# Kernel optimization log

Hardware: AMD Instinct MI355X
Metric: run time of the kernel (lower is better)

The kernel has to match this reference:

```python
import jax, jax.numpy as jnp
import numpy as np

N_NODES = 100000
N_EDGES = 800000
NUM_FEATURES = 64
HIDDEN = 16
N_GRAPHS = 64


def setup_inputs() -> dict:
    key = jax.random.key(0)
    ks = jax.random.split(key, 12)
    x = jax.random.normal(ks[0], (N_NODES, NUM_FEATURES), dtype=jnp.float32)
    edge_index = jax.random.randint(ks[1], (2, N_EDGES), 0, N_NODES, dtype=jnp.int64)
    batch = jnp.sort(jax.random.randint(ks[2], (N_NODES,), 0, N_GRAPHS, dtype=jnp.int64))
    def glorot(k, shape):
        fan_in, fan_out = shape
        s = jnp.sqrt(2.0 / (fan_in + fan_out))
        return jax.random.normal(k, shape, dtype=jnp.float32) * s
    return {
        "x": x,
        "edge_index": edge_index,
        "batch": batch,
        "W1_rel": glorot(ks[3], (NUM_FEATURES, HIDDEN)),
        "W1_root": glorot(ks[4], (NUM_FEATURES, HIDDEN)),
        "b1": jnp.zeros((HIDDEN,), dtype=jnp.float32),
        "W2_rel": glorot(ks[5], (HIDDEN, HIDDEN)),
        "W2_root": glorot(ks[6], (HIDDEN, HIDDEN)),
        "b2": jnp.zeros((HIDDEN,), dtype=jnp.float32),
        "Wlin": glorot(ks[7], (HIDDEN, 1)),
        "blin": jnp.zeros((1,), dtype=jnp.float32),
    }


def _graph_conv(h, src, dst, W_rel, W_root, b):
    # PyG GraphConv: out_i = W_rel @ sum_{j->i} h_j + b + W_root @ h_i
    agg = jax.ops.segment_sum(h[src], dst, num_segments=h.shape[0])
    return agg @ W_rel + b + h @ W_root


def reference(x, edge_index, batch, W1_rel, W1_root, b1, W2_rel, W2_root, b2, Wlin, blin):
    src, dst = edge_index[0], edge_index[1]
    h = jax.nn.relu(_graph_conv(x, src, dst, W1_rel, W1_root, b1))
    # F.dropout(training=False) is identity at inference
    h = _graph_conv(h, src, dst, W2_rel, W2_root, b2)
    # global mean pool over graphs
    sums = jax.ops.segment_sum(h, batch, num_segments=N_GRAPHS)  # [G, H]
    counts = jax.ops.segment_sum(jnp.ones((h.shape[0],), dtype=h.dtype), batch, num_segments=N_GRAPHS)
    pooled = sums / jnp.maximum(counts, 1.0)[:, None]
    out = pooled @ Wlin + blin  # [G, 1]
    return out.squeeze(1)
```

## Files before the change

kernel.cpp:

```cpp
#include <hip/hip_runtime.h>

#define BUCKET_BITS 7
#define BUCKET_N    128
#define SEG_CAP     1280
#define EPB         4096
#define EPT         16
#define OVF_CAP     16384
#define MAXBUCK     1024

__global__ void k_init(int* __restrict__ cursor, int* __restrict__ ovf_n,
                       float* __restrict__ T1, float* __restrict__ T2,
                       float* __restrict__ cntg, int nbuck, int n_graphs)
{
    const int t = threadIdx.x;
    for (int i = t; i < nbuck; i += 1024) cursor[i * 16] = i * SEG_CAP;
    if (t < n_graphs) { T1[t] = 0.f; T2[t] = 0.f; cntg[t] = 0.f; }
    if (t == 0) *ovf_n = 0;
}

__global__ __launch_bounds__(256) void k_scatter_bin(
    const int* __restrict__ src, const int* __restrict__ dst,
    int* __restrict__ cursor, int2* __restrict__ seg,
    int* __restrict__ ovf_n, int2* __restrict__ ovf,
    int n_edges, int nbuck)
{
    __shared__ int hist[MAXBUCK];
    __shared__ int base[MAXBUCK];
    const int t = threadIdx.x;
    for (int i = t; i < nbuck; i += 256) hist[i] = 0;
    __syncthreads();

    const int e0 = blockIdx.x * EPB;
    int es[EPT], ed[EPT], ep[EPT];
#pragma unroll
    for (int k = 0; k < EPT; ++k) {
        const int e = e0 + k * 256 + t;
        if (e < n_edges) {
            ed[k] = dst[e];
            es[k] = src[e];
            ep[k] = atomicAdd(&hist[ed[k] >> BUCKET_BITS], 1);
        } else ed[k] = -1;
    }
    __syncthreads();
    for (int b = t; b < nbuck; b += 256) {
        const int h = hist[b];
        base[b] = h ? atomicAdd(&cursor[b * 16], h) : 0;
    }
    __syncthreads();
#pragma unroll
    for (int k = 0; k < EPT; ++k) {
        if (ed[k] >= 0) {
            const int b = ed[k] >> BUCKET_BITS;
            const int addr = base[b] + ep[k];
            if (addr < (b + 1) * SEG_CAP) {
                seg[addr] = make_int2(es[k], ed[k]);
            } else {
                const int op = atomicAdd(ovf_n, 1);
                if (op < OVF_CAP) ovf[op] = make_int2(es[k], ed[k]);
            }
        }
    }
}

__global__ __launch_bounds__(256) void k_transform1(
    const float* __restrict__ x, const float* __restrict__ Wrel,
    const float* __restrict__ Wroot, const float* __restrict__ bias,
    float* __restrict__ p1, float* __restrict__ r1, int n_nodes)
{
    __shared__ float s_x[64 * 68];
    __shared__ float s_wrT[16 * 68];
    __shared__ float s_woT[16 * 68];
    __shared__ float s_b[16];

    const int t = threadIdx.x;
    for (int i = t; i < 1024; i += 256) {
        const int k = i >> 4, o = i & 15;
        s_wrT[o * 68 + k] = Wrel[i];
        s_woT[o * 68 + k] = Wroot[i];
    }
    if (t < 16) s_b[t] = bias[t];

    const int node0 = blockIdx.x * 64;
    for (int i = t; i < 1024; i += 256) {
        const int r = i >> 4, c = i & 15;
        const int node = node0 + r;
        if (node < n_nodes)
            *(float4*)&s_x[r * 68 + c * 4] =
                *(const float4*)(x + (size_t)node * 64 + c * 4);
    }
    __syncthreads();

    const int o = t & 15, ng = t >> 4;
    float accr[4] = {0.f, 0.f, 0.f, 0.f};
    float acco[4] = {0.f, 0.f, 0.f, 0.f};
#pragma unroll
    for (int k4 = 0; k4 < 16; ++k4) {
        const float4 wr = *(const float4*)&s_wrT[o * 68 + k4 * 4];
        const float4 wo = *(const float4*)&s_woT[o * 68 + k4 * 4];
#pragma unroll
        for (int j = 0; j < 4; ++j) {
            const float4 xv = *(const float4*)&s_x[(ng * 4 + j) * 68 + k4 * 4];
            accr[j] = fmaf(xv.x, wr.x, fmaf(xv.y, wr.y, fmaf(xv.z, wr.z, fmaf(xv.w, wr.w, accr[j]))));
            acco[j] = fmaf(xv.x, wo.x, fmaf(xv.y, wo.y, fmaf(xv.z, wo.z, fmaf(xv.w, wo.w, acco[j]))));
        }
    }
#pragma unroll
    for (int j = 0; j < 4; ++j) {
        const int node = node0 + ng * 4 + j;
        if (node < n_nodes) {
            p1[(size_t)node * 16 + o] = accr[j];
            r1[(size_t)node * 16 + o] = acco[j] + s_b[o];
        }
    }
}

__global__ __launch_bounds__(256) void k_aggregate(
    const float* __restrict__ p1, const float* __restrict__ r1,
    const int2* __restrict__ seg, const int* __restrict__ cursor,
    const int* __restrict__ ovf_n, const int2* __restrict__ ovf,
    const int* __restrict__ batch,
    const float* __restrict__ W2rel, const float* __restrict__ W2root,
    const float* __restrict__ Wlin,
    float* __restrict__ s_out, float* __restrict__ T2, float* __restrict__ cntg,
    int* __restrict__ g_sorted, int* __restrict__ g_beg, int* __restrict__ g_cnt,
    int n_nodes)
{
    __shared__ int s_src[SEG_CAP];
    __shared__ int hist[BUCKET_N];
    __shared__ int iscan[BUCKET_N];
    __shared__ int cur[BUCKET_N];
    __shared__ float s_w2r[16], s_w2o[16];
    __shared__ float sT2[64], scnt[64];
    __shared__ int s_no;

    const int t = threadIdx.x, b = blockIdx.x;
    if (t < BUCKET_N) hist[t] = 0;
    if (t < 16) {
        float ar = 0.f, ao = 0.f;
#pragma unroll
        for (int o = 0; o < 16; ++o) {
            const float wl = Wlin[o];
            ar = fmaf(W2rel[t * 16 + o], wl, ar);
            ao = fmaf(W2root[t * 16 + o], wl, ao);
        }
        s_w2r[t] = ar; s_w2o[t] = ao;
    }
    if (t < 64) { sT2[t] = 0.f; scnt[t] = 0.f; }
    if (t == 0) s_no = min(*ovf_n, OVF_CAP);
    __syncthreads();

    const int bstart = b * SEG_CAP;
    const int count = min(cursor[b * 16] - bstart, SEG_CAP);

    for (int i = t; i < count; i += 256)
        atomicAdd(&hist[seg[bstart + i].y & (BUCKET_N - 1)], 1);
    __syncthreads();
    if (t < BUCKET_N) iscan[t] = hist[t];
    __syncthreads();
    for (int off = 1; off < BUCKET_N; off <<= 1) {
        int x = 0;
        if (t < BUCKET_N) { x = iscan[t]; if (t >= off) x += iscan[t - off]; }
        __syncthreads();
        if (t < BUCKET_N) iscan[t] = x;
        __syncthreads();
    }
    if (t < BUCKET_N) cur[t] = iscan[t] - hist[t];
    __syncthreads();
    for (int i = t; i < count; i += 256) {
        const int2 e = seg[bstart + i];
        const int l = e.y & (BUCKET_N - 1);
        s_src[atomicAdd(&cur[l], 1)] = e.x;
    }
    __syncthreads();

    for (int i = t; i < count; i += 256) g_sorted[bstart + i] = s_src[i];
    if (t < BUCKET_N) {
        const int nodew = b * BUCKET_N + t;
        if (nodew < n_nodes) {
            g_beg[nodew] = bstart + iscan[t] - hist[t];
            g_cnt[nodew] = hist[t];
        }
    }

    const int nl = t >> 1, half = t & 1;
    const int node = b * BUCKET_N + nl;
    if (node < n_nodes) {
        const int end = iscan[nl];
        const int beg = end - hist[nl];
        float4 acc0 = make_float4(0.f, 0.f, 0.f, 0.f);
        float4 acc1 = make_float4(0.f, 0.f, 0.f, 0.f);
        int j = beg;
        for (; j + 2 <= end; j += 2) {
            const int s0 = s_src[j], s1 = s_src[j + 1];
            const float4* q0 = (const float4*)(p1 + (size_t)s0 * 16 + half * 8);
            const float4* q1 = (const float4*)(p1 + (size_t)s1 * 16 + half * 8);
            const float4 a0 = q0[0], a1 = q0[1], b0 = q1[0], b1 = q1[1];
            acc0.x += a0.x + b0.x; acc0.y += a0.y + b0.y;
            acc0.z += a0.z + b0.z; acc0.w += a0.w + b0.w;
            acc1.x += a1.x + b1.x; acc1.y += a1.y + b1.y;
            acc1.z += a1.z + b1.z; acc1.w += a1.w + b1.w;
        }
        if (j < end) {
            const int s0 = s_src[j];
            const float4* q0 = (const float4*)(p1 + (size_t)s0 * 16 + half * 8);
            const float4 a0 = q0[0], a1 = q0[1];
            acc0.x += a0.x; acc0.y += a0.y; acc0.z += a0.z; acc0.w += a0.w;
            acc1.x += a1.x; acc1.y += a1.y; acc1.z += a1.z; acc1.w += a1.w;
        }
        for (int ov = 0; ov < s_no; ++ov) {
            const int2 e = ovf[ov];
            if (e.y == node) {
                const float4* q0 = (const float4*)(p1 + (size_t)e.x * 16 + half * 8);
                const float4 a0 = q0[0], a1 = q0[1];
                acc0.x += a0.x; acc0.y += a0.y; acc0.z += a0.z; acc0.w += a0.w;
                acc1.x += a1.x; acc1.y += a1.y; acc1.z += a1.z; acc1.w += a1.w;
            }
        }
        const float4 rA = *(const float4*)(r1 + (size_t)node * 16 + half * 8);
        const float4 rB = *(const float4*)(r1 + (size_t)node * 16 + half * 8 + 4);
        float4 h0, h1;
        h0.x = fmaxf(acc0.x + rA.x, 0.f); h0.y = fmaxf(acc0.y + rA.y, 0.f);
        h0.z = fmaxf(acc0.z + rA.z, 0.f); h0.w = fmaxf(acc0.w + rA.w, 0.f);
        h1.x = fmaxf(acc1.x + rB.x, 0.f); h1.y = fmaxf(acc1.y + rB.y, 0.f);
        h1.z = fmaxf(acc1.z + rB.z, 0.f); h1.w = fmaxf(acc1.w + rB.w, 0.f);
        const float4 w0r = *(const float4*)&s_w2r[half * 8];
        const float4 w1r = *(const float4*)&s_w2r[half * 8 + 4];
        const float4 w0o = *(const float4*)&s_w2o[half * 8];
        const float4 w1o = *(const float4*)&s_w2o[half * 8 + 4];
        float ps = h0.x * w0r.x + h0.y * w0r.y + h0.z * w0r.z + h0.w * w0r.w
                 + h1.x * w1r.x + h1.y * w1r.y + h1.z * w1r.z + h1.w * w1r.w;
        float pu = h0.x * w0o.x + h0.y * w0o.y + h0.z * w0o.z + h0.w * w0o.w
                 + h1.x * w1o.x + h1.y * w1o.y + h1.z * w1o.z + h1.w * w1o.w;
        ps += __shfl_xor(ps, 1);
        pu += __shfl_xor(pu, 1);
        if (half == 0) {
            s_out[node] = ps;
            const int g = batch[node];
            atomicAdd(&sT2[g], pu);
            atomicAdd(&scnt[g], 1.f);
        }
    }
    __syncthreads();
    if (t < 64) {
        if (sT2[t] != 0.f) unsafeAtomicAdd(&T2[t], sT2[t]);
        if (scnt[t] != 0.f) unsafeAtomicAdd(&cntg[t], scnt[t]);
    }
}

__global__ __launch_bounds__(256) void k_T1(
    const float* __restrict__ s_in, const int* __restrict__ g_sorted,
    const int* __restrict__ g_beg, const int* __restrict__ g_cnt,
    const int* __restrict__ batch,
    const int* __restrict__ ovf_n, const int2* __restrict__ ovf,
    float* __restrict__ T1, int n_nodes)
{
    __shared__ float bins[64];
    const int t = threadIdx.x;
    if (t < 64) bins[t] = 0.f;
    __syncthreads();

    const int node = blockIdx.x * 256 + t;
    if (node < n_nodes) {
        const int beg = g_beg[node], c = g_cnt[node];
        float acc = 0.f;
        int j = 0;
        for (; j + 4 <= c; j += 4) {
            const int a = g_sorted[beg + j],     b2 = g_sorted[beg + j + 1];
            const int cc = g_sorted[beg + j + 2], d = g_sorted[beg + j + 3];
            acc += s_in[a] + s_in[b2] + s_in[cc] + s_in[d];
        }
        for (; j < c; ++j) acc += s_in[g_sorted[beg + j]];
        if (acc != 0.f) atomicAdd(&bins[batch[node]], acc);
    }
    __syncthreads();
    if (t < 64 && bins[t] != 0.f) unsafeAtomicAdd(&T1[t], bins[t]);

    if (blockIdx.x == 0) {
        const int n = min(*ovf_n, OVF_CAP);
        for (int i = t; i < n; i += 256)
            unsafeAtomicAdd(&T1[batch[ovf[i].y]], s_in[ovf[i].x]);
    }
}

__global__ void k_finalize(
    const float* __restrict__ T1, const float* __restrict__ T2,
    const float* __restrict__ cntg, const float* __restrict__ b2,
    const float* __restrict__ Wlin, const float* __restrict__ blin,
    float* __restrict__ out, int n_graphs)
{
    const int g = threadIdx.x;
    if (g >= n_graphs) return;
    float cb = 0.f;
#pragma unroll
    for (int o = 0; o < 16; ++o) cb = fmaf(b2[o], Wlin[o], cb);
    const float c = fmaxf(cntg[g], 1.f);
    out[g] = (T1[g] + T2[g]) / c + cb + blin[0];
}

extern "C" void kernel_launch(void* const* d_in, const int* in_sizes, int n_in,
                              void* d_out, int out_size, void* d_ws, size_t ws_size,
                              hipStream_t stream) {
    const float* x       = (const float*)d_in[0];
    const int*   ei      = (const int*)d_in[1];
    const int*   batch   = (const int*)d_in[2];
    const float* W1_rel  = (const float*)d_in[3];
    const float* W1_root = (const float*)d_in[4];
    const float* b1      = (const float*)d_in[5];
    const float* W2_rel  = (const float*)d_in[6];
    const float* W2_root = (const float*)d_in[7];
    const float* b2      = (const float*)d_in[8];
    const float* Wlin    = (const float*)d_in[9];
    const float* blin    = (const float*)d_in[10];
    float* out = (float*)d_out;

    const int N = in_sizes[0] / 64;
    const int E = in_sizes[1] / 2;
    const int G = out_size;
    const int nbuck = (N + BUCKET_N - 1) >> BUCKET_BITS;

    const int* src = ei;
    const int* dst = ei + E;

    auto rnd4 = [](size_t v) { return (v + 3) & ~(size_t)3; };
    float* ws = (float*)d_ws;
    size_t off = 0;
    float* p1       = ws + off; off += rnd4((size_t)N * 16);
    float* r1       = ws + off; off += rnd4((size_t)N * 16);
    float* s_buf    = ws + off; off += rnd4((size_t)N);
    int*   cursor   = (int*)(ws + off); off += rnd4((size_t)nbuck * 16);
    int2*  seg      = (int2*)(ws + off); off += rnd4((size_t)nbuck * SEG_CAP * 2);
    int*   g_sorted = (int*)(ws + off); off += rnd4((size_t)nbuck * SEG_CAP);
    int*   g_beg    = (int*)(ws + off); off += rnd4((size_t)N);
    int*   g_cnt    = (int*)(ws + off); off += rnd4((size_t)N);
    int2*  ovf      = (int2*)(ws + off); off += rnd4((size_t)OVF_CAP * 2);
    int*   ovf_n    = (int*)(ws + off); off += 4;
    float* T1       = ws + off; off += rnd4((size_t)G);
    float* T2       = ws + off; off += rnd4((size_t)G);
    float* cntg     = ws + off; off += rnd4((size_t)G);

    const int sb = (E + EPB - 1) / EPB;
    const int tb = (N + 63) / 64;
    const int ab = (N + 255) / 256;

    k_init       <<<1, 1024, 0, stream>>>(cursor, ovf_n, T1, T2, cntg, nbuck, G);
    k_scatter_bin<<<sb, 256, 0, stream>>>(src, dst, cursor, seg, ovf_n, ovf, E, nbuck);
    k_transform1 <<<tb, 256, 0, stream>>>(x, W1_rel, W1_root, b1, p1, r1, N);
    k_aggregate  <<<nbuck, 256, 0, stream>>>(p1, r1, seg, cursor, ovf_n, ovf, batch,
                                             W2_rel, W2_root, Wlin, s_buf, T2, cntg,
                                             g_sorted, g_beg, g_cnt, N);
    k_T1         <<<ab, 256, 0, stream>>>(s_buf, g_sorted, g_beg, g_cnt, batch,
                                          ovf_n, ovf, T1, N);
    k_finalize   <<<1, 64, 0, stream>>>(T1, T2, cntg, b2, Wlin, blin, out, G);
}
```

Measured before the change: 169.3 us.

## Store projected features in fp16, cache edges in registers, use wave-shuffle scan

The projected layer-1 features p1 are now stored as half precision, which halves the bytes of the random gather in the aggregation kernel, and are widened to fp32 for accumulation. The aggregation kernel also keeps its edges in registers between the histogram and placement passes, avoiding a second read of the segment. It replaces the shared-memory Hillis-Steele scan with a wavefront shuffle scan. The init kernel is split across 8 blocks. fp16 rounding of p1 adds numerical error to the result.

```diff
diff --git a/kernel.cpp b/kernel.cpp
--- a/kernel.cpp
+++ b/kernel.cpp
@@ -1,4 +1,5 @@
 #include <hip/hip_runtime.h>
+#include <hip/hip_fp16.h>
 
 #define BUCKET_BITS 7
 #define BUCKET_N    128
@@ -8,14 +9,18 @@
 #define OVF_CAP     16384
 #define MAXBUCK     1024
 
-__global__ void k_init(int* __restrict__ cursor, int* __restrict__ ovf_n,
-                       float* __restrict__ T1, float* __restrict__ T2,
-                       float* __restrict__ cntg, int nbuck, int n_graphs)
-{
-    const int t = threadIdx.x;
-    for (int i = t; i < nbuck; i += 1024) cursor[i * 16] = i * SEG_CAP;
-    if (t < n_graphs) { T1[t] = 0.f; T2[t] = 0.f; cntg[t] = 0.f; }
-    if (t == 0) *ovf_n = 0;
+__global__ __launch_bounds__(256) void k_init(
+    int* __restrict__ cursor, int* __restrict__ ovf_n,
+    float* __restrict__ T1, float* __restrict__ T2,
+    float* __restrict__ cntg, int nbuck, int n_graphs)
+{
+    const int i0 = blockIdx.x * 256 + threadIdx.x;
+    for (int i = i0; i < nbuck; i += gridDim.x * 256) cursor[i * 16] = i * SEG_CAP;
+    if (blockIdx.x == 0) {
+        const int t = threadIdx.x;
+        if (t < n_graphs) { T1[t] = 0.f; T2[t] = 0.f; cntg[t] = 0.f; }
+        if (t == 0) *ovf_n = 0;
+    }
 }
 
 __global__ __launch_bounds__(256) void k_scatter_bin(
@@ -65,7 +70,7 @@
 __global__ __launch_bounds__(256) void k_transform1(
     const float* __restrict__ x, const float* __restrict__ Wrel,
     const float* __restrict__ Wroot, const float* __restrict__ bias,
-    float* __restrict__ p1, float* __restrict__ r1, int n_nodes)
+    __half* __restrict__ p1, float* __restrict__ r1, int n_nodes)
 {
     __shared__ float s_x[64 * 68];
     __shared__ float s_wrT[16 * 68];
@@ -108,14 +113,24 @@
     for (int j = 0; j < 4; ++j) {
         const int node = node0 + ng * 4 + j;
         if (node < n_nodes) {
-            p1[(size_t)node * 16 + o] = accr[j];
+            p1[(size_t)node * 16 + o] = __float2half(accr[j]);
             r1[(size_t)node * 16 + o] = acco[j] + s_b[o];
         }
     }
 }
 
+__device__ inline void acc_half8(float* acc, uint4 raw) {
+    const __half2* h2 = (const __half2*)&raw;
+#pragma unroll
+    for (int k = 0; k < 4; ++k) {
+        const float2 f = __half22float2(h2[k]);
+        acc[2 * k]     += f.x;
+        acc[2 * k + 1] += f.y;
+    }
+}
+
 __global__ __launch_bounds__(256) void k_aggregate(
-    const float* __restrict__ p1, const float* __restrict__ r1,
+    const __half* __restrict__ p1, const float* __restrict__ r1,
     const int2* __restrict__ seg, const int* __restrict__ cursor,
     const int* __restrict__ ovf_n, const int2* __restrict__ ovf,
     const int* __restrict__ batch,
@@ -131,7 +146,7 @@
     __shared__ int cur[BUCKET_N];
     __shared__ float s_w2r[16], s_w2o[16];
     __shared__ float sT2[64], scnt[64];
-    __shared__ int s_no;
+    __shared__ int s_no, s_w0;
 
     const int t = threadIdx.x, b = blockIdx.x;
     if (t < BUCKET_N) hist[t] = 0;
@@ -152,25 +167,33 @@
     const int bstart = b * SEG_CAP;
     const int count = min(cursor[b * 16] - bstart, SEG_CAP);
 
-    for (int i = t; i < count; i += 256)
-        atomicAdd(&hist[seg[bstart + i].y & (BUCKET_N - 1)], 1);
-    __syncthreads();
-    if (t < BUCKET_N) iscan[t] = hist[t];
-    __syncthreads();
-    for (int off = 1; off < BUCKET_N; off <<= 1) {
-        int x = 0;
-        if (t < BUCKET_N) { x = iscan[t]; if (t >= off) x += iscan[t - off]; }
-        __syncthreads();
-        if (t < BUCKET_N) iscan[t] = x;
-        __syncthreads();
-    }
-    if (t < BUCKET_N) cur[t] = iscan[t] - hist[t];
-    __syncthreads();
+    int2 er[5];
+    int ne = 0;
     for (int i = t; i < count; i += 256) {
-        const int2 e = seg[bstart + i];
-        const int l = e.y & (BUCKET_N - 1);
-        s_src[atomicAdd(&cur[l], 1)] = e.x;
-    }
+        er[ne] = seg[bstart + i];
+        atomicAdd(&hist[er[ne].y & (BUCKET_N - 1)], 1);
+        ++ne;
+    }
+    __syncthreads();
+    int v = 0;
+    if (t < BUCKET_N) {
+        v = hist[t];
+#pragma unroll
+        for (int off = 1; off < 64; off <<= 1) {
+            const int u = __shfl_up(v, off);
+            if ((t & 63) >= off) v += u;
+        }
+        if (t == 63) s_w0 = v;
+    }
+    __syncthreads();
+    if (t < BUCKET_N) {
+        if (t >= 64) v += s_w0;
+        iscan[t] = v;
+        cur[t] = v - hist[t];
+    }
+    __syncthreads();
+    for (int k = 0; k < ne; ++k)
+        s_src[atomicAdd(&cur[er[k].y & (BUCKET_N - 1)], 1)] = er[k].x;
     __syncthreads();
 
     for (int i = t; i < count; i += 256) g_sorted[bstart + i] = s_src[i];
@@ -187,50 +210,39 @@
     if (node < n_nodes) {
         const int end = iscan[nl];
         const int beg = end - hist[nl];
-        float4 acc0 = make_float4(0.f, 0.f, 0.f, 0.f);
-        float4 acc1 = make_float4(0.f, 0.f, 0.f, 0.f);
+        float acc[8] = {0.f, 0.f, 0.f, 0.f, 0.f, 0.f, 0.f, 0.f};
         int j = beg;
         for (; j + 2 <= end; j += 2) {
             const int s0 = s_src[j], s1 = s_src[j + 1];
-            const float4* q0 = (const float4*)(p1 + (size_t)s0 * 16 + half * 8);
-            const float4* q1 = (const float4*)(p1 + (size_t)s1 * 16 + half * 8);
-            const float4 a0 = q0[0], a1 = q0[1], b0 = q1[0], b1 = q1[1];
-            acc0.x += a0.x + b0.x; acc0.y += a0.y + b0.y;
-            acc0.z += a0.z + b0.z; acc0.w += a0.w + b0.w;
-            acc1.x += a1.x + b1.x; acc1.y += a1.y + b1.y;
-            acc1.z += a1.z + b1.z; acc1.w += a1.w + b1.w;
+            const uint4 a = *(const uint4*)(p1 + (size_t)s0 * 16 + half * 8);
+            const uint4 c = *(const uint4*)(p1 + (size_t)s1 * 16 + half * 8);
+            acc_half8(acc, a);
+            acc_half8(acc, c);
         }
         if (j < end) {
-            const int s0 = s_src[j];
-            const float4* q0 = (const float4*)(p1 + (size_t)s0 * 16 + half * 8);
-            const float4 a0 = q0[0], a1 = q0[1];
-            acc0.x += a0.x; acc0.y += a0.y; acc0.z += a0.z; acc0.w += a0.w;
-            acc1.x += a1.x; acc1.y += a1.y; acc1.z += a1.z; acc1.w += a1.w;
+            const uint4 a = *(const uint4*)(p1 + (size_t)s_src[j] * 16 + half * 8);
+            acc_half8(acc, a);
         }
         for (int ov = 0; ov < s_no; ++ov) {
             const int2 e = ovf[ov];
             if (e.y == node) {
-                const float4* q0 = (const float4*)(p1 + (size_t)e.x * 16 + half * 8);
-                const float4 a0 = q0[0], a1 = q0[1];
-                acc0.x += a0.x; acc0.y += a0.y; acc0.z += a0.z; acc0.w += a0.w;
-                acc1.x += a1.x; acc1.y += a1.y; acc1.z += a1.z; acc1.w += a1.w;
+                const uint4 a = *(const uint4*)(p1 + (size_t)e.x * 16 + half * 8);
+                acc_half8(acc, a);
             }
         }
         const float4 rA = *(const float4*)(r1 + (size_t)node * 16 + half * 8);
         const float4 rB = *(const float4*)(r1 + (size_t)node * 16 + half * 8 + 4);
-        float4 h0, h1;
-        h0.x = fmaxf(acc0.x + rA.x, 0.f); h0.y = fmaxf(acc0.y + rA.y, 0.f);
-        h0.z = fmaxf(acc0.z + rA.z, 0.f); h0.w = fmaxf(acc0.w + rA.w, 0.f);
-        h1.x = fmaxf(acc1.x + rB.x, 0.f); h1.y = fmaxf(acc1.y + rB.y, 0.f);
-        h1.z = fmaxf(acc1.z + rB.z, 0.f); h1.w = fmaxf(acc1.w + rB.w, 0.f);
-        const float4 w0r = *(const float4*)&s_w2r[half * 8];
-        const float4 w1r = *(const float4*)&s_w2r[half * 8 + 4];
-        const float4 w0o = *(const float4*)&s_w2o[half * 8];
-        const float4 w1o = *(const float4*)&s_w2o[half * 8 + 4];
-        float ps = h0.x * w0r.x + h0.y * w0r.y + h0.z * w0r.z + h0.w * w0r.w
-                 + h1.x * w1r.x + h1.y * w1r.y + h1.z * w1r.z + h1.w * w1r.w;
-        float pu = h0.x * w0o.x + h0.y * w0o.y + h0.z * w0o.z + h0.w * w0o.w
-                 + h1.x * w1o.x + h1.y * w1o.y + h1.z * w1o.z + h1.w * w1o.w;
+        float h[8];
+        h[0] = fmaxf(acc[0] + rA.x, 0.f); h[1] = fmaxf(acc[1] + rA.y, 0.f);
+        h[2] = fmaxf(acc[2] + rA.z, 0.f); h[3] = fmaxf(acc[3] + rA.w, 0.f);
+        h[4] = fmaxf(acc[4] + rB.x, 0.f); h[5] = fmaxf(acc[5] + rB.y, 0.f);
+        h[6] = fmaxf(acc[6] + rB.z, 0.f); h[7] = fmaxf(acc[7] + rB.w, 0.f);
+        float ps = 0.f, pu = 0.f;
+#pragma unroll
+        for (int k = 0; k < 8; ++k) {
+            ps = fmaf(h[k], s_w2r[half * 8 + k], ps);
+            pu = fmaf(h[k], s_w2o[half * 8 + k], pu);
+        }
         ps += __shfl_xor(ps, 1);
         pu += __shfl_xor(pu, 1);
         if (half == 0) {
@@ -265,7 +277,7 @@
         float acc = 0.f;
         int j = 0;
         for (; j + 4 <= c; j += 4) {
-            const int a = g_sorted[beg + j],     b2 = g_sorted[beg + j + 1];
+            const int a = g_sorted[beg + j],      b2 = g_sorted[beg + j + 1];
             const int cc = g_sorted[beg + j + 2], d = g_sorted[beg + j + 3];
             acc += s_in[a] + s_in[b2] + s_in[cc] + s_in[d];
         }
@@ -324,7 +336,7 @@
     auto rnd4 = [](size_t v) { return (v + 3) & ~(size_t)3; };
     float* ws = (float*)d_ws;
     size_t off = 0;
-    float* p1       = ws + off; off += rnd4((size_t)N * 16);
+    __half* p1      = (__half*)(ws + off); off += rnd4((size_t)N * 8);
     float* r1       = ws + off; off += rnd4((size_t)N * 16);
     float* s_buf    = ws + off; off += rnd4((size_t)N);
     int*   cursor   = (int*)(ws + off); off += rnd4((size_t)nbuck * 16);
@@ -342,7 +354,7 @@
     const int tb = (N + 63) / 64;
     const int ab = (N + 255) / 256;
 
-    k_init       <<<1, 1024, 0, stream>>>(cursor, ovf_n, T1, T2, cntg, nbuck, G);
+    k_init       <<<8, 256, 0, stream>>>(cursor, ovf_n, T1, T2, cntg, nbuck, G);
     k_scatter_bin<<<sb, 256, 0, stream>>>(src, dst, cursor, seg, ovf_n, ovf, E, nbuck);
     k_transform1 <<<tb, 256, 0, stream>>>(x, W1_rel, W1_root, b1, p1, r1, N);
     k_aggregate  <<<nbuck, 256, 0, stream>>>(p1, r1, seg, cursor, ovf_n, ovf, batch,
```

Result: slower. 182.2 us (+7.6%).
